# Kernel tuning notes

Measured on AMD Instinct MI355X. Metric: run time of the kernel, lower is better.

Reference implementation:

```python
import jax, jax.numpy as jnp
import numpy as np

A = -0.75  # torch bicubic coefficient
K = 5
K2 = K * K
IN_CH = 32 * 2 + 169 + 16 * 2 + 1  # 266
TIMESTEP = 0.5


def _cubic_w(t):
    # t in [0,1); weights for taps at offsets -1,0,1,2 (torch cubic convolution, A=-0.75)
    w1 = ((A + 2.0) * t - (A + 3.0)) * t * t + 1.0
    s = 1.0 - t
    w2 = ((A + 2.0) * s - (A + 3.0)) * s * s + 1.0
    u = t + 1.0
    w0 = ((A * u - 5.0 * A) * u + 8.0 * A) * u - 4.0 * A
    v = 2.0 - t
    w3 = ((A * v - 5.0 * A) * v + 8.0 * A) * v - 4.0 * A
    return (w0, w1, w2, w3)


def _conv3(x, w, b):
    y = jax.lax.conv_general_dilated(x, w, (1, 1), 'SAME',
                                     dimension_numbers=('NCHW', 'OIHW', 'NCHW'))
    return y + b[None, :, None, None]


def _lrelu(x):
    return jnp.where(x >= 0, x, 0.1 * x)


def _kernel_pred(x, w1, b1, w2, b2, w3, b3, ow, ob, ww, wb):
    f = _lrelu(_conv3(x, w1, b1))
    f = _lrelu(_conv3(f, w2, b2))
    f = _lrelu(_conv3(f, w3, b3))
    offsets = _conv3(f, ow, ob)                      # (B, 2*K2, H, W)
    weights = jax.nn.softmax(_conv3(f, ww, wb), axis=1)  # (B, K2, H, W)
    return offsets, weights


def _adacof_sample(image, offsets, weights):
    # bicubic grid_sample(padding_mode='border', align_corners=True) + weighted combine
    b, c, h, w = image.shape
    k2 = weights.shape[1]
    gx = jnp.arange(w, dtype=image.dtype)
    gy = jnp.arange(h, dtype=image.dtype)
    dx = offsets[:, 0::2]                # (b,k2,h,w)
    dy = offsets[:, 1::2]
    # with align_corners=True, normalize->unnormalize is identity
    sx = gx[None, None, None, :] + dx
    sy = gy[None, None, :, None] + dy
    x0 = jnp.floor(sx); tx = sx - x0
    y0 = jnp.floor(sy); ty = sy - y0
    wx = _cubic_w(tx)
    wy = _cubic_w(ty)
    xi = [jnp.clip(x0 + (i - 1.0), 0, w - 1).astype(jnp.int32) for i in range(4)]
    yi = [jnp.clip(y0 + (i - 1.0), 0, h - 1).astype(jnp.int32) for i in range(4)]
    imgf = image.reshape(b, c, h * w)
    gather = jax.vmap(lambda im, idx: im[:, idx])   # (c,hw),(n,)->(c,n)
    acc = jnp.zeros((b, c, k2, h, w), image.dtype)
    for i in range(4):
        for j in range(4):
            idx = (yi[i] * w + xi[j]).reshape(b, -1)
            g = gather(imgf, idx).reshape(b, c, k2, h, w)
            acc = acc + g * (wy[i] * wx[j])[:, None]
    return jnp.einsum('bckhw,bkhw->bchw', acc, weights)


def setup_inputs() -> dict:
    key = jax.random.key(0)
    ks = iter(jax.random.split(key, 64))
    d = {}
    d['frame1'] = jax.random.normal(next(ks), (2, 3, 256, 256), jnp.float32)
    d['frame2'] = jax.random.normal(next(ks), (2, 3, 256, 256), jnp.float32)
    d['feat1'] = jax.random.normal(next(ks), (2, 32, 256, 256), jnp.float32)
    d['feat2'] = jax.random.normal(next(ks), (2, 32, 256, 256), jnp.float32)
    d['corr'] = jax.random.normal(next(ks), (2, 169, 256, 256), jnp.float32)

    def conv_w(o, i):
        return jax.random.normal(next(ks), (o, i, 3, 3), jnp.float32) * 0.05

    # full-res encoder
    d['fr_w1'] = conv_w(16, 3); d['fr_b1'] = jnp.zeros((16,), jnp.float32)
    d['fr_w2'] = conv_w(16, 16); d['fr_b2'] = jnp.zeros((16,), jnp.float32)
    # default grid offsets for offset_head bias (dx,dy interleaved)
    off_bias = []
    for i in range(K):
        for j in range(K):
            off_bias.extend([j - K // 2, i - K // 2])
    off_bias = jnp.asarray(off_bias, jnp.float32)
    for p in ('kp1', 'kp2'):
        d[p + '_w1'] = conv_w(256, IN_CH); d[p + '_b1'] = jnp.zeros((256,), jnp.float32)
        d[p + '_w2'] = conv_w(256, 256); d[p + '_b2'] = jnp.zeros((256,), jnp.float32)
        d[p + '_w3'] = conv_w(128, 256); d[p + '_b3'] = jnp.zeros((128,), jnp.float32)
        d[p + '_ow'] = jax.random.normal(next(ks), (2 * K2, 128, 3, 3), jnp.float32) * 0.01
        d[p + '_ob'] = off_bias
        d[p + '_ww'] = jax.random.normal(next(ks), (K2, 128, 3, 3), jnp.float32) * 0.01
        d[p + '_wb'] = jnp.full((K2,), 1.0 / K2, jnp.float32)
    d['bl_w1'] = conv_w(64, IN_CH); d['bl_b1'] = jnp.zeros((64,), jnp.float32)
    d['bl_w2'] = conv_w(1, 64); d['bl_b2'] = jnp.zeros((1,), jnp.float32)
    return d


def reference(frame1, frame2, feat1, feat2, corr,
              fr_w1, fr_b1, fr_w2, fr_b2,
              kp1_w1, kp1_b1, kp1_w2, kp1_b2, kp1_w3, kp1_b3, kp1_ow, kp1_ob, kp1_ww, kp1_wb,
              kp2_w1, kp2_b1, kp2_w2, kp2_b2, kp2_w3, kp2_b3, kp2_ow, kp2_ob, kp2_ww, kp2_wb,
              bl_w1, bl_b1, bl_w2, bl_b2):
    b, _, h, w = frame1.shape
    fr1 = _lrelu(_conv3(_lrelu(_conv3(frame1, fr_w1, fr_b1)), fr_w2, fr_b2))
    fr2 = _lrelu(_conv3(_lrelu(_conv3(frame2, fr_w1, fr_b1)), fr_w2, fr_b2))
    t_map = jnp.full((b, 1, h, w), TIMESTEP, frame1.dtype)
    combined = jnp.concatenate([feat1, feat2, corr, fr1, fr2, t_map], axis=1)
    offsets1, weights1 = _kernel_pred(combined, kp1_w1, kp1_b1, kp1_w2, kp1_b2,
                                      kp1_w3, kp1_b3, kp1_ow, kp1_ob, kp1_ww, kp1_wb)
    offsets2, weights2 = _kernel_pred(combined, kp2_w1, kp2_b1, kp2_w2, kp2_b2,
                                      kp2_w3, kp2_b3, kp2_ow, kp2_ob, kp2_ww, kp2_wb)
    sample1 = _adacof_sample(frame1, offsets1, weights1)
    sample2 = _adacof_sample(frame2, offsets2, weights2)
    blend = jax.nn.sigmoid(_conv3(_lrelu(_conv3(combined, bl_w1, bl_b1)), bl_w2, bl_b2))
    output = blend * sample1 + (1.0 - blend) * sample2
    return (output, blend, offsets1, offsets2, weights1, weights2)
```

## Files before the change

kernel.cpp:

```cpp
#include <hip/hip_runtime.h>
#include <cstdint>
#include <cstddef>

#define H 256
#define W 256
#define HW (H*W)
#define BATCH 2
#define CIN_TILE 4

typedef __bf16 bf16x8 __attribute__((ext_vector_type(8)));
typedef float f32x4 __attribute__((ext_vector_type(4)));
typedef __attribute__((address_space(1))) uint32_t gu32_t;
typedef __attribute__((address_space(3))) uint32_t lu32_t;

__device__ __forceinline__ void async16(const void* g, void* l) {
  __builtin_amdgcn_global_load_lds((const gu32_t*)g, (lu32_t*)l, 16, 0, 0);
}

__device__ __forceinline__ ushort f2bf(float f) {
  uint u = __float_as_uint(f);
  return (ushort)((u + 0x7FFFu + ((u >> 16) & 1u)) >> 16);
}
__device__ __forceinline__ float lrelu_f(float v) { return v >= 0.f ? v : 0.1f * v; }

#define SWN (2304 * 8)
#define SBN (4 * 640 * 8)
#define DYN_LDS_BYTES (2 * (SWN + SBN) * 2)

template<int EPI>
__global__ __launch_bounds__(512) void convmm_k(
    const ushort* __restrict__ act, const ushort* __restrict__ wgt,
    const float* __restrict__ bias, ushort* __restrict__ dstb,
    float* __restrict__ dsto, float* __restrict__ dstw,
    const ushort* __restrict__ zpage, int Cin, int CoutS,
    int astride, int wstride, int bstride, int dstride)
{
  extern __shared__ __align__(16) ushort s_dyn[];

  const int z = blockIdx.z;
  act += (size_t)z * astride;
  wgt += (size_t)z * wstride;
  bias += (size_t)z * bstride;
  if constexpr (EPI == 0) dstb += (size_t)z * dstride;
  else { dsto += (size_t)z * (BATCH * 50 * HW); dstw += (size_t)z * (BATCH * 25 * HW); }

  const int tid = threadIdx.x;
  const int sp = blockIdx.x;
  const int bx = (sp & 7) * 32, by = (sp >> 3) * 16;
  const int co0 = blockIdx.y * 64;
  const int wv = tid >> 6, lane = tid & 63;
  const int c = lane & 15, kq = lane >> 4;
  const int oy = wv * 2;

  int wsrc[5];
#pragma unroll
  for (int it = 0; it < 5; ++it) {
    int i = tid + it * 512;
    if (i < 2304) {
      int co = i & 63, tk = i >> 6, tap = tk >> 2, kg = tk & 3;
      wsrc[it] = ((co0 + co) * 9 + tap) * Cin + kg * 8;
    } else wsrc[it] = 0;
  }
  int bsrc[5];
#pragma unroll
  for (int it = 0; it < 5; ++it) {
    int i = tid + it * 512;
    int kg = i / 640, px = i - kg * 640;
    int row = px / 34, xx = px - row * 34;
    int gy = by + row - 1, gx = bx + xx - 1;
    bool ok = (px < 612) && ((unsigned)gy < (unsigned)H) && ((unsigned)gx < (unsigned)W);
    bsrc[it] = ok ? ((gy * W + gx) * Cin + kg * 8) : -1;
  }

  auto stage = [&](int buf, int c0) {
    ushort* swc = s_dyn + (buf ? (SWN + SBN) : 0);
    ushort* sbc = swc + SWN;
#pragma unroll
    for (int it = 0; it < 5; ++it)
      if (it < 4 || tid < 2304 - 4 * 512)
        async16(wgt + wsrc[it] + c0, &swc[(size_t)(tid + it * 512) * 8]);
#pragma unroll
    for (int it = 0; it < 5; ++it) {
      const ushort* g = (bsrc[it] < 0) ? zpage : (act + bsrc[it] + c0);
      async16(g, &sbc[(size_t)(tid + it * 512) * 8]);
    }
  };

  f32x4 acc[4][4];
#pragma unroll
  for (int a = 0; a < 4; ++a)
#pragma unroll
    for (int b2 = 0; b2 < 4; ++b2) acc[a][b2] = (f32x4){0.f, 0.f, 0.f, 0.f};

  stage(0, 0);
  __syncthreads();

  const int nch = Cin >> 5;
  int cur = 0;
  for (int ch = 0; ch < nch; ++ch) {
    if (ch + 1 < nch) stage(cur ^ 1, (ch + 1) << 5);

    const ushort* swc = s_dyn + (cur ? (SWN + SBN) : 0);
    const ushort* sbc = swc + SWN;

#pragma unroll
    for (int t = 0; t < 9; ++t) {
      const int dy = t / 3 - 1, dx = t % 3 - 1;
      bf16x8 B[4];
#pragma unroll
      for (int pf = 0; pf < 4; ++pf) {
        int p = (oy + (pf >> 1) + dy + 1) * 34 + (pf & 1) * 16 + dx + 1 + c;
        B[pf] = *(const bf16x8*)&sbc[(size_t)(kq * 640 + p) * 8];
      }
#pragma unroll
      for (int cf = 0; cf < 4; ++cf) {
        bf16x8 A = *(const bf16x8*)&swc[(size_t)((t * 4 + kq) * 64 + cf * 16 + c) * 8];
#pragma unroll
        for (int pf = 0; pf < 4; ++pf)
          acc[cf][pf] = __builtin_amdgcn_mfma_f32_16x16x32_bf16(A, B[pf], acc[cf][pf], 0, 0, 0);
      }
    }

    __syncthreads();
    cur ^= 1;
  }

  const int r4 = kq * 4;
#pragma unroll
  for (int cf = 0; cf < 4; ++cf) {
    int cob = co0 + cf * 16 + r4;
#pragma unroll
    for (int pf = 0; pf < 4; ++pf) {
      int gx2 = bx + (pf & 1) * 16 + c;
      int gy2 = by + oy + (pf >> 1);
      int gpix = gy2 * W + gx2;
      f32x4 v = acc[cf][pf];
      const float4 bv = *(const float4*)&bias[cob];
      if constexpr (EPI == 0) {
        ushort4 ov;
        float f0 = lrelu_f(v[0] + bv.x);
        float f1 = lrelu_f(v[1] + bv.y);
        float f2 = lrelu_f(v[2] + bv.z);
        float f3 = lrelu_f(v[3] + bv.w);
        ov.x = f2bf(f0); ov.y = f2bf(f1); ov.z = f2bf(f2); ov.w = f2bf(f3);
        *(ushort4*)&dstb[(size_t)gpix * CoutS + cob] = ov;
      } else {
        const float* bvp = &bv.x;
#pragma unroll
        for (int r = 0; r < 4; ++r) {
          int coa = cob + r;
          if (coa < 75) {
            float f = v[r] + bvp[r];
            if (coa < 50) dsto[(size_t)coa * HW + gpix] = f;
            else          dstw[(size_t)(coa - 50) * HW + gpix] = f;
          }
        }
      }
    }
  }
}

template<int CIN>
__global__ __launch_bounds__(256) void conv_fr_k(
    const float* __restrict__ sA, const float* __restrict__ sB, int mode,
    const float* __restrict__ wgt, const float* __restrict__ bias,
    float* __restrict__ dst)
{
  const int z = blockIdx.y;
  const float* src = (mode == 0)
      ? (((z >> 1) ? sB : sA) + (size_t)(z & 1) * 3 * HW)
      : (sA + (size_t)z * 16 * HW);
  float* out = dst + (size_t)z * 16 * HW;

  const int sp = blockIdx.x;
  const int bx = (sp & 7) * 32, by = (sp >> 3) * 32;
  const int tid = threadIdx.x;
  const int tx = tid & 15, ty = tid >> 4;

  __shared__ float s_in[CIN_TILE][34][36];
  float acc[16][2][2];
#pragma unroll
  for (int co = 0; co < 16; ++co) {
    acc[co][0][0] = 0.f; acc[co][0][1] = 0.f;
    acc[co][1][0] = 0.f; acc[co][1][1] = 0.f;
  }

  for (int c0 = 0; c0 < CIN; c0 += CIN_TILE) {
    __syncthreads();
    const int nst = CIN_TILE * 34 * 34;
    for (int i = tid; i < nst; i += 256) {
      int ci = i / (34 * 34);
      int r = i - ci * (34 * 34);
      int yy = r / 34;
      int xx = r - yy * 34;
      int gy = by + yy - 1, gx = bx + xx - 1;
      int cc = c0 + ci;
      float v = 0.f;
      if (cc < CIN && (unsigned)gy < (unsigned)H && (unsigned)gx < (unsigned)W)
        v = src[(size_t)cc * HW + gy * W + gx];
      s_in[ci][yy][xx] = v;
    }
    __syncthreads();

    const int cmax = (CIN - c0 < CIN_TILE) ? (CIN - c0) : CIN_TILE;
    for (int ci = 0; ci < cmax; ++ci) {
      float win[4][4];
#pragma unroll
      for (int iy = 0; iy < 4; ++iy)
#pragma unroll
        for (int ix = 0; ix < 4; ++ix)
          win[iy][ix] = s_in[ci][2 * ty + iy][2 * tx + ix];
#pragma unroll
      for (int co = 0; co < 16; ++co) {
        const float* wp = wgt + ((size_t)co * CIN + (c0 + ci)) * 9;
        float w0 = wp[0], w1 = wp[1], w2 = wp[2];
        float w3 = wp[3], w4 = wp[4], w5 = wp[5];
        float w6 = wp[6], w7 = wp[7], w8 = wp[8];
#pragma unroll
        for (int py = 0; py < 2; ++py)
#pragma unroll
          for (int px = 0; px < 2; ++px) {
            float s = acc[co][py][px];
            s += w0 * win[py + 0][px + 0];
            s += w1 * win[py + 0][px + 1];
            s += w2 * win[py + 0][px + 2];
            s += w3 * win[py + 1][px + 0];
            s += w4 * win[py + 1][px + 1];
            s += w5 * win[py + 1][px + 2];
            s += w6 * win[py + 2][px + 0];
            s += w7 * win[py + 2][px + 1];
            s += w8 * win[py + 2][px + 2];
            acc[co][py][px] = s;
          }
      }
    }
  }
#pragma unroll
  for (int co = 0; co < 16; ++co) {
    float bv = bias[co];
#pragma unroll
    for (int py = 0; py < 2; ++py)
#pragma unroll
      for (int px = 0; px < 2; ++px)
        out[(size_t)co * HW + (size_t)(by + 2 * ty + py) * W + (bx + 2 * tx + px)] =
            lrelu_f(acc[co][py][px] + bv);
  }
}

__global__ __launch_bounds__(256) void pack_k(
    const float* __restrict__ feat1, const float* __restrict__ feat2,
    const float* __restrict__ corr, const float* __restrict__ fr,
    ushort* __restrict__ comb, int b)
{
  int gid = blockIdx.x * 256 + threadIdx.x;
  int chunk = gid / HW;
  int p = gid - chunk * HW;
  int c0 = chunk * 32;

  uint u[16];
#pragma unroll
  for (int j = 0; j < 32; j += 2) {
    float f[2];
#pragma unroll
    for (int q = 0; q < 2; ++q) {
      int cc = c0 + j + q;
      float v;
      if (cc < 32)       v = feat1[(size_t)(b * 32 + cc) * HW + p];
      else if (cc < 64)  v = feat2[(size_t)(b * 32 + cc - 32) * HW + p];
      else if (cc < 233) v = corr[(size_t)(b * 169 + cc - 64) * HW + p];
      else if (cc < 249) v = fr[(size_t)(b * 16 + (cc - 233)) * HW + p];
      else if (cc < 265) v = fr[(size_t)((2 + b) * 16 + (cc - 249)) * HW + p];
      else if (cc == 265) v = 0.5f;
      else               v = 0.f;
      f[q] = v;
    }
    u[j >> 1] = (uint)f2bf(f[0]) | ((uint)f2bf(f[1]) << 16);
  }
  uint4* dst = (uint4*)&comb[(size_t)p * 288 + c0];
#pragma unroll
  for (int q = 0; q < 4; ++q) {
    uint4 t;
    t.x = u[q * 4 + 0]; t.y = u[q * 4 + 1]; t.z = u[q * 4 + 2]; t.w = u[q * 4 + 3];
    dst[q] = t;
  }
}

struct PrepSeg { const float* src; ushort* dst; int O, I, Ipad; };
struct PrepArgs { PrepSeg s[13]; int pre[14]; };

__global__ __launch_bounds__(256) void prep_all_k(PrepArgs a)
{
  int gid = blockIdx.x * 256 + threadIdx.x;
  if (gid >= a.pre[13]) return;
  int si = 0;
  while (gid >= a.pre[si + 1]) ++si;
  int idx = gid - a.pre[si];
  const PrepSeg sg = a.s[si];
  int i = idx % sg.Ipad;
  int r = idx / sg.Ipad;
  int tap = r % 9;
  int o = r / 9;
  float v = (i < sg.I) ? sg.src[((size_t)o * sg.I + i) * 9 + tap] : 0.f;
  sg.dst[idx] = f2bf(v);
}

__global__ __launch_bounds__(256) void bias_all_k(
    const float* kb1_0, const float* kb1_1, const float* kb2_0, const float* kb2_1,
    const float* kb3_0, const float* kb3_1,
    const float* ob0, const float* wb0, const float* ob1, const float* wb1,
    float* bb1, float* bb2, float* bb3, float* bbh)
{
  int yq = blockIdx.y;
  int i = threadIdx.x;
  switch (yq) {
    case 0: bb1[i] = kb1_0[i]; break;
    case 1: bb1[256 + i] = kb1_1[i]; break;
    case 2: bb2[i] = kb2_0[i]; break;
    case 3: bb2[256 + i] = kb2_1[i]; break;
    case 4: if (i < 128) bb3[i] = kb3_0[i]; break;
    case 5: if (i < 128) bb3[128 + i] = kb3_1[i]; break;
    case 6: if (i < 128) bbh[i]       = (i < 50) ? ob0[i] : ((i < 75) ? wb0[i - 50] : 0.f); break;
    case 7: if (i < 128) bbh[128 + i] = (i < 50) ? ob1[i] : ((i < 75) ? wb1[i - 50] : 0.f); break;
  }
}

__global__ __launch_bounds__(256) void blend2_k(
    const ushort* __restrict__ actD, const float* __restrict__ wgt,
    const float* __restrict__ b2, float* __restrict__ outp)
{
  int p = blockIdx.x * 256 + threadIdx.x;
  int y = p >> 8, x = p & 255;
  float acc = b2[0];
  for (int dy = -1; dy <= 1; ++dy) {
    int gy = y + dy;
    if ((unsigned)gy >= (unsigned)H) continue;
    for (int dx = -1; dx <= 1; ++dx) {
      int gx = x + dx;
      if ((unsigned)gx >= (unsigned)W) continue;
      int tap = (dy + 1) * 3 + (dx + 1);
      const ushort* rowp = actD + (size_t)(gy * W + gx) * 64;
#pragma unroll
      for (int c8 = 0; c8 < 8; ++c8) {
        uint4 v = *(const uint4*)&rowp[c8 * 8];
        const uint* vv = &v.x;
#pragma unroll
        for (int q = 0; q < 4; ++q) {
          float f0 = __uint_as_float(vv[q] << 16);
          float f1 = __uint_as_float(vv[q] & 0xFFFF0000u);
          int ci = c8 * 8 + q * 2;
          acc += f0 * wgt[ci * 9 + tap];
          acc += f1 * wgt[(ci + 1) * 9 + tap];
        }
      }
    }
  }
  outp[p] = 1.f / (1.f + expf(-acc));
}

__global__ __launch_bounds__(256) void softmax25_k(float* __restrict__ w1,
                                                   float* __restrict__ w2)
{
  float* wr = blockIdx.y ? w2 : w1;
  int p = blockIdx.x * 256 + threadIdx.x;
  if (p >= HW) return;
  float v[25];
  float m = -1e30f;
#pragma unroll
  for (int k = 0; k < 25; ++k) {
    v[k] = wr[(size_t)k * HW + p];
    m = fmaxf(m, v[k]);
  }
  float s = 0.f;
#pragma unroll
  for (int k = 0; k < 25; ++k) {
    v[k] = expf(v[k] - m);
    s += v[k];
  }
  float inv = 1.f / s;
#pragma unroll
  for (int k = 0; k < 25; ++k)
    wr[(size_t)k * HW + p] = v[k] * inv;
}

__device__ __forceinline__ void cubic4(float t, float* cw)
{
  const float A_ = -0.75f;
  float t2 = t * t;
  cw[1] = ((A_ + 2.f) * t - (A_ + 3.f)) * t2 + 1.f;
  float s = 1.f - t;
  cw[2] = ((A_ + 2.f) * s - (A_ + 3.f)) * (s * s) + 1.f;
  float u = t + 1.f;
  cw[0] = ((A_ * u - 5.f * A_) * u + 8.f * A_) * u - 4.f * A_;
  float v = 2.f - t;
  cw[3] = ((A_ * v - 5.f * A_) * v + 8.f * A_) * v - 4.f * A_;
}

#define ATW 64
#define ATH 4
#define AHL 8
#define AROWS (ATH + 2*AHL)
#define ACOLS (ATW + 2*AHL)

__global__ __launch_bounds__(256) void adacof_final_k(
    const float* __restrict__ frame1, const float* __restrict__ frame2,
    const float* __restrict__ off1, const float* __restrict__ off2,
    const float* __restrict__ wt1, const float* __restrict__ wt2,
    const float* __restrict__ blend, float* __restrict__ outp)
{
  __shared__ __align__(16) float4 s_img[2 * AROWS * ACOLS];

  const int tid = threadIdx.x;
  int t = blockIdx.x;
  const int tilesPerImg = (H / ATH) * (W / ATW);
  const int b = t / tilesPerImg; t -= b * tilesPerImg;
  const int by = (t >> 2) * ATH, bx = (t & 3) * ATW;
  const int ty = tid >> 6, txx = tid & 63;
  const int y = by + ty, x = bx + txx;
  const int p = y * W + x;
  const int tx0 = bx - AHL, ty0 = by - AHL;

  const float* f1 = frame1 + (size_t)b * 3 * HW;
  const float* f2 = frame2 + (size_t)b * 3 * HW;

  for (int i = tid; i < AROWS * ACOLS; i += 256) {
    int r = i / ACOLS, cc = i - r * ACOLS;
    int gy = min(max(ty0 + r, 0), H - 1);
    int gx = min(max(tx0 + cc, 0), W - 1);
    int q = gy * W + gx;
    float4 v1, v2;
    v1.x = f1[q]; v1.y = f1[HW + q]; v1.z = f1[2 * HW + q]; v1.w = 0.f;
    v2.x = f2[q]; v2.y = f2[HW + q]; v2.z = f2[2 * HW + q]; v2.w = 0.f;
    s_img[i] = v1;
    s_img[AROWS * ACOLS + i] = v2;
  }
  __syncthreads();

  float a1[3] = {0.f, 0.f, 0.f};
  float a2[3] = {0.f, 0.f, 0.f};

  const size_t ob1 = (size_t)b * 50 * HW, wb1 = (size_t)b * 25 * HW;

#pragma unroll 2
  for (int k = 0; k < 25; ++k) {
#pragma unroll
    for (int fr = 0; fr < 2; ++fr) {
      const float* off = fr ? off2 : off1;
      const float* wts = fr ? wt2 : wt1;
      const float* img = fr ? f2 : f1;
      float* acc = fr ? a2 : a1;

      float dx = off[ob1 + (size_t)(2 * k) * HW + p];
      float dy = off[ob1 + (size_t)(2 * k + 1) * HW + p];
      float wk = wts[wb1 + (size_t)k * HW + p];
      float sx = (float)x + dx, sy = (float)y + dy;
      float x0f = floorf(sx), y0f = floorf(sy);
      float tx = sx - x0f, tyf = sy - y0f;
      float wx[4], wy[4];
      cubic4(tx, wx);
      cubic4(tyf, wy);
      int ix0 = (int)x0f, iy0 = (int)y0f;

      bool inT = (ix0 - 1 >= tx0) && (ix0 + 2 <= tx0 + ACOLS - 1) &&
                 (iy0 - 1 >= ty0) && (iy0 + 2 <= ty0 + AROWS - 1);
      if (__builtin_expect(inT, 1)) {
        const float4* base = &s_img[(size_t)fr * AROWS * ACOLS +
                                    (iy0 - 1 - ty0) * ACOLS + (ix0 - 1 - tx0)];
#pragma unroll
        for (int i = 0; i < 4; ++i) {
#pragma unroll
          for (int j = 0; j < 4; ++j) {
            float wf = wy[i] * wx[j] * wk;
            float4 v = base[i * ACOLS + j];
            acc[0] += v.x * wf;
            acc[1] += v.y * wf;
            acc[2] += v.z * wf;
          }
        }
      } else {
        int xi[4], yi[4];
#pragma unroll
        for (int i = 0; i < 4; ++i) {
          xi[i] = min(max(ix0 + i - 1, 0), W - 1);
          yi[i] = min(max(iy0 + i - 1, 0), H - 1);
        }
#pragma unroll
        for (int i = 0; i < 4; ++i) {
#pragma unroll
          for (int j = 0; j < 4; ++j) {
            float wf = wy[i] * wx[j] * wk;
            int q = yi[i] * W + xi[j];
            acc[0] += img[q] * wf;
            acc[1] += img[HW + q] * wf;
            acc[2] += img[2 * HW + q] * wf;
          }
        }
      }
    }
  }

  float bl = blend[(size_t)b * HW + p];
#pragma unroll
  for (int c3 = 0; c3 < 3; ++c3)
    outp[((size_t)b * 3 + c3) * HW + p] = bl * a1[c3] + (1.f - bl) * a2[c3];
}

extern "C" void kernel_launch(void* const* d_in, const int* in_sizes, int n_in,
                              void* d_out, int out_size, void* d_ws, size_t ws_size,
                              hipStream_t stream)
{
  const float* frame1 = (const float*)d_in[0];
  const float* frame2 = (const float*)d_in[1];
  const float* feat1  = (const float*)d_in[2];
  const float* feat2  = (const float*)d_in[3];
  const float* corr   = (const float*)d_in[4];
  const float* fr_w1  = (const float*)d_in[5];
  const float* fr_b1  = (const float*)d_in[6];
  const float* fr_w2  = (const float*)d_in[7];
  const float* fr_b2  = (const float*)d_in[8];

  const float* kw1[2] = {(const float*)d_in[9],  (const float*)d_in[19]};
  const float* kb1[2] = {(const float*)d_in[10], (const float*)d_in[20]};
  const float* kw2[2] = {(const float*)d_in[11], (const float*)d_in[21]};
  const float* kb2[2] = {(const float*)d_in[12], (const float*)d_in[22]};
  const float* kw3[2] = {(const float*)d_in[13], (const float*)d_in[23]};
  const float* kb3[2] = {(const float*)d_in[14], (const float*)d_in[24]};
  const float* kow[2] = {(const float*)d_in[15], (const float*)d_in[25]};
  const float* kob[2] = {(const float*)d_in[16], (const float*)d_in[26]};
  const float* kww[2] = {(const float*)d_in[17], (const float*)d_in[27]};
  const float* kwb[2] = {(const float*)d_in[18], (const float*)d_in[28]};

  const float* bl_w1 = (const float*)d_in[29];
  const float* bl_b1 = (const float*)d_in[30];
  const float* bl_w2 = (const float*)d_in[31];
  const float* bl_b2 = (const float*)d_in[32];

  float* out = (float*)d_out;
  float* o_out   = out;
  float* o_blend = o_out   + (size_t)BATCH * 3 * HW;
  float* o_off1  = o_blend + (size_t)BATCH * 1 * HW;
  float* o_off2  = o_off1  + (size_t)BATCH * 50 * HW;
  float* o_w1    = o_off2  + (size_t)BATCH * 50 * HW;
  float* o_w2    = o_w1    + (size_t)BATCH * 25 * HW;

  hipFuncSetAttribute((const void*)convmm_k<0>,
                      hipFuncAttributeMaxDynamicSharedMemorySize, DYN_LDS_BYTES);
  hipFuncSetAttribute((const void*)convmm_k<1>,
                      hipFuncAttributeMaxDynamicSharedMemorySize, DYN_LDS_BYTES);

  size_t off = 0;
  char* wsb = (char*)d_ws;
  auto alloc = [&](size_t bytes) -> void* {
    void* pp = wsb + off;
    off += (bytes + 255) & ~(size_t)255;
    return pp;
  };
  const size_t NEED_MERGED = 212700000;
  const bool merged = ws_size >= NEED_MERGED;
  const int NZ = merged ? 2 : 1;

  ushort* zpage = (ushort*)alloc(512);
  ushort* wp1   = (ushort*)alloc((size_t)2 * 256 * 9 * 288 * 2);
  ushort* wp2   = (ushort*)alloc((size_t)2 * 256 * 9 * 256 * 2);
  ushort* wp3   = (ushort*)alloc((size_t)2 * 128 * 9 * 256 * 2);
  ushort* wph   = (ushort*)alloc((size_t)2 * 128 * 9 * 128 * 2);
  ushort* wpb   = (ushort*)alloc((size_t)64 * 9 * 288 * 2);
  float*  bb1   = (float*)alloc(2 * 256 * 4);
  float*  bb2   = (float*)alloc(2 * 256 * 4);
  float*  bb3   = (float*)alloc(2 * 128 * 4);
  float*  bbh   = (float*)alloc(2 * 128 * 4);
  float*  tmp4  = (float*)alloc((size_t)4 * 16 * HW * 4);
  float*  frbuf = (float*)alloc((size_t)4 * 16 * HW * 4);
  ushort* comb  = (ushort*)alloc((size_t)HW * 288 * 2);
  ushort* actA  = (ushort*)alloc((size_t)NZ * HW * 256 * 2);
  ushort* actB  = (ushort*)alloc((size_t)NZ * HW * 256 * 2);

  dim3 blk(256);
  dim3 cblk(512);

  hipMemsetAsync(zpage, 0, 512, stream);
  {
    PrepArgs pa;
    const int W1 = 256 * 9 * 288, W2 = 256 * 9 * 256, W3 = 128 * 9 * 256;
    const int OW = 50 * 9 * 128, WW = 25 * 9 * 128, ZW = 53 * 9 * 128;
    const int WB = 64 * 9 * 288;
    const int HP = 128 * 9 * 128;
    PrepSeg segs[13] = {
      {kw1[0], wp1,                    256, 266, 288},
      {kw1[1], wp1 + W1,               256, 266, 288},
      {kw2[0], wp2,                    256, 256, 256},
      {kw2[1], wp2 + W2,               256, 256, 256},
      {kw3[0], wp3,                    128, 256, 256},
      {kw3[1], wp3 + W3,               128, 256, 256},
      {kow[0], wph,                     50, 128, 128},
      {kww[0], wph + OW,                25, 128, 128},
      {nullptr, wph + OW + WW,          53,   0, 128},
      {kow[1], wph + HP,                50, 128, 128},
      {kww[1], wph + HP + OW,           25, 128, 128},
      {nullptr, wph + HP + OW + WW,     53,   0, 128},
      {bl_w1,  wpb,                     64, 266, 288},
    };
    int tots[13] = {W1, W1, W2, W2, W3, W3, OW, WW, ZW, OW, WW, ZW, WB};
    pa.pre[0] = 0;
    for (int s = 0; s < 13; ++s) { pa.s[s] = segs[s]; pa.pre[s + 1] = pa.pre[s] + tots[s]; }
    int nblk = (pa.pre[13] + 255) / 256;
    prep_all_k<<<dim3(nblk), blk, 0, stream>>>(pa);
  }
  bias_all_k<<<dim3(1, 8), blk, 0, stream>>>(kb1[0], kb1[1], kb2[0], kb2[1],
                                             kb3[0], kb3[1], kob[0], kwb[0],
                                             kob[1], kwb[1], bb1, bb2, bb3, bbh);

  conv_fr_k<3><<<dim3(64, 4), blk, 0, stream>>>(frame1, frame2, 0, fr_w1, fr_b1, tmp4);
  conv_fr_k<16><<<dim3(64, 4), blk, 0, stream>>>(tmp4, nullptr, 1, fr_w2, fr_b2, frbuf);

  const int W1 = 256 * 9 * 288, W2 = 256 * 9 * 256, W3 = 128 * 9 * 256;
  const int HP = 128 * 9 * 128;

  for (int b = 0; b < BATCH; ++b) {
    pack_k<<<dim3(9 * HW / 256), blk, 0, stream>>>(feat1, feat2, corr, frbuf, comb, b);

    for (int pp = 0; pp < 2 / NZ; ++pp) {
      const size_t po = pp;
      convmm_k<0><<<dim3(128, 4, NZ), cblk, DYN_LDS_BYTES, stream>>>(
          comb, wp1 + po * W1, bb1 + po * 256, actA + po * (size_t)HW * 256,
          nullptr, nullptr, zpage, 288, 256, 0, W1, 256, HW * 256);
      convmm_k<0><<<dim3(128, 4, NZ), cblk, DYN_LDS_BYTES, stream>>>(
          actA + po * (size_t)HW * 256, wp2 + po * W2, bb2 + po * 256,
          actB + po * (size_t)HW * 256,
          nullptr, nullptr, zpage, 256, 256, HW * 256, W2, 256, HW * 256);
      convmm_k<0><<<dim3(128, 2, NZ), cblk, DYN_LDS_BYTES, stream>>>(
          actB + po * (size_t)HW * 256, wp3 + po * W3, bb3 + po * 128,
          actA + po * (size_t)HW * 128,
          nullptr, nullptr, zpage, 256, 128, HW * 256, W3, 128, HW * 128);
      convmm_k<1><<<dim3(128, 2, NZ), cblk, DYN_LDS_BYTES, stream>>>(
          actA + po * (size_t)HW * 128, wph + po * HP, bbh + po * 128, nullptr,
          o_off1 + (size_t)b * 50 * HW + po * (size_t)BATCH * 50 * HW,
          o_w1 + (size_t)b * 25 * HW + po * (size_t)BATCH * 25 * HW,
          zpage, 128, 0, HW * 128, HP, 128, 0);
    }
    softmax25_k<<<dim3(HW / 256, 2), blk, 0, stream>>>(
        o_w1 + (size_t)b * 25 * HW, o_w2 + (size_t)b * 25 * HW);

    convmm_k<0><<<dim3(128, 1, 1), cblk, DYN_LDS_BYTES, stream>>>(
        comb, wpb, bl_b1, actB, nullptr, nullptr, zpage, 288, 64, 0, 0, 0, 0);
    blend2_k<<<dim3(HW / 256), blk, 0, stream>>>(actB, bl_w2, bl_b2,
                                                 o_blend + (size_t)b * HW);
  }

  adacof_final_k<<<dim3(BATCH * (H / ATH) * (W / ATW)), blk, 0, stream>>>(
      frame1, frame2, o_off1, o_off2, o_w1, o_w2, o_blend, o_out);
}
```

Before: 1.331 ms.

## Software-pipeline LDS fragment reads across taps with inline asm and setprio

Replaces the compiler-scheduled LDS loads in the conv implicit-GEMM inner loop with hand-issued ds_read_b128 instructions. They use precomputed base addresses and immediate tap offsets, and the A/B fragments are double-buffered in registers so the reads for tap t+1 are in flight while the MFMAs for tap t run. Manual lgkmcnt waits and sched_barriers enforce the ordering, and s_setprio raises wave priority around the MFMA burst. The aim is to hide LDS latency and cut address arithmetic. The cost is higher register pressure and fragile manual synchronization that the compiler can no longer reorder.

```diff
diff --git a/kernel.cpp b/kernel.cpp
--- a/kernel.cpp
+++ b/kernel.cpp
@@ -26,6 +26,30 @@
 #define SWN (2304 * 8)
 #define SBN (4 * 640 * 8)
 #define DYN_LDS_BYTES (2 * (SWN + SBN) * 2)
+
+#define ISSUE_TAP(tt, bb)                                                     \
+  do {                                                                        \
+    asm volatile("ds_read_b128 %0, %1 offset:%c2"                             \
+                 : "=v"(Afr[bb][0]) : "v"(aA0), "i"((tt) * 4096));            \
+    asm volatile("ds_read_b128 %0, %1 offset:%c2"                             \
+                 : "=v"(Afr[bb][1]) : "v"(aA1), "i"((tt) * 4096));            \
+    asm volatile("ds_read_b128 %0, %1 offset:%c2"                             \
+                 : "=v"(Afr[bb][2]) : "v"(aA2), "i"((tt) * 4096));            \
+    asm volatile("ds_read_b128 %0, %1 offset:%c2"                             \
+                 : "=v"(Afr[bb][3]) : "v"(aA3), "i"((tt) * 4096));            \
+    asm volatile("ds_read_b128 %0, %1 offset:%c2"                             \
+                 : "=v"(Bfr[bb][0]) : "v"(aB0),                               \
+                   "i"(((((tt) / 3) * 34) + ((tt) % 3)) * 16));               \
+    asm volatile("ds_read_b128 %0, %1 offset:%c2"                             \
+                 : "=v"(Bfr[bb][1]) : "v"(aB1),                               \
+                   "i"(((((tt) / 3) * 34) + ((tt) % 3)) * 16));               \
+    asm volatile("ds_read_b128 %0, %1 offset:%c2"                             \
+                 : "=v"(Bfr[bb][2]) : "v"(aB2),                               \
+                   "i"(((((tt) / 3) * 34) + ((tt) % 3)) * 16));               \
+    asm volatile("ds_read_b128 %0, %1 offset:%c2"                             \
+                 : "=v"(Bfr[bb][3]) : "v"(aB3),                               \
+                   "i"(((((tt) / 3) * 34) + ((tt) % 3)) * 16));               \
+  } while (0)
 
 template<int EPI>
 __global__ __launch_bounds__(512) void convmm_k(
@@ -95,30 +119,56 @@
   stage(0, 0);
   __syncthreads();
 
+  const uint sdyn_base = (uint)(uintptr_t)(lu32_t*)s_dyn;
+
   const int nch = Cin >> 5;
   int cur = 0;
   for (int ch = 0; ch < nch; ++ch) {
     if (ch + 1 < nch) stage(cur ^ 1, (ch + 1) << 5);
-
-    const ushort* swc = s_dyn + (cur ? (SWN + SBN) : 0);
-    const ushort* sbc = swc + SWN;
+    __builtin_amdgcn_sched_barrier(0);
+
+    const uint swoff = sdyn_base + (cur ? (uint)((SWN + SBN) * 2) : 0u);
+    const uint sboff = swoff + (uint)(SWN * 2);
+    const uint aA0 = swoff + (uint)((kq * 64 + 0 * 16 + c) * 16);
+    const uint aA1 = swoff + (uint)((kq * 64 + 1 * 16 + c) * 16);
+    const uint aA2 = swoff + (uint)((kq * 64 + 2 * 16 + c) * 16);
+    const uint aA3 = swoff + (uint)((kq * 64 + 3 * 16 + c) * 16);
+    const uint aB0 = sboff + (uint)((kq * 640 + (oy + 0) * 34 + 0 * 16 + c) * 16);
+    const uint aB1 = sboff + (uint)((kq * 640 + (oy + 0) * 34 + 1 * 16 + c) * 16);
+    const uint aB2 = sboff + (uint)((kq * 640 + (oy + 1) * 34 + 0 * 16 + c) * 16);
+    const uint aB3 = sboff + (uint)((kq * 640 + (oy + 1) * 34 + 1 * 16 + c) * 16);
+
+    bf16x8 Afr[2][4], Bfr[2][4];
+    ISSUE_TAP(0, 0);
 
 #pragma unroll
     for (int t = 0; t < 9; ++t) {
-      const int dy = t / 3 - 1, dx = t % 3 - 1;
-      bf16x8 B[4];
-#pragma unroll
-      for (int pf = 0; pf < 4; ++pf) {
-        int p = (oy + (pf >> 1) + dy + 1) * 34 + (pf & 1) * 16 + dx + 1 + c;
-        B[pf] = *(const bf16x8*)&sbc[(size_t)(kq * 640 + p) * 8];
+      if (t < 8) {
+        switch (t + 1) {
+          case 1: ISSUE_TAP(1, 1); break;
+          case 2: ISSUE_TAP(2, 0); break;
+          case 3: ISSUE_TAP(3, 1); break;
+          case 4: ISSUE_TAP(4, 0); break;
+          case 5: ISSUE_TAP(5, 1); break;
+          case 6: ISSUE_TAP(6, 0); break;
+          case 7: ISSUE_TAP(7, 1); break;
+          case 8: ISSUE_TAP(8, 0); break;
+        }
+        asm volatile("s_waitcnt lgkmcnt(8)" ::: "memory");
+      } else {
+        asm volatile("s_waitcnt lgkmcnt(0)" ::: "memory");
       }
+      __builtin_amdgcn_sched_barrier(0);
+      __builtin_amdgcn_s_setprio(1);
 #pragma unroll
       for (int cf = 0; cf < 4; ++cf) {
-        bf16x8 A = *(const bf16x8*)&swc[(size_t)((t * 4 + kq) * 64 + cf * 16 + c) * 8];
 #pragma unroll
         for (int pf = 0; pf < 4; ++pf)
-          acc[cf][pf] = __builtin_amdgcn_mfma_f32_16x16x32_bf16(A, B[pf], acc[cf][pf], 0, 0, 0);
+          acc[cf][pf] = __builtin_amdgcn_mfma_f32_16x16x32_bf16(
+              Afr[t & 1][cf], Bfr[t & 1][pf], acc[cf][pf], 0, 0, 0);
       }
+      __builtin_amdgcn_s_setprio(0);
+      __builtin_amdgcn_sched_barrier(0);
     }
 
     __syncthreads();
```

Result: faster. 1.302 ms (median of 2 runs) (-2.2%).

## Widen conv implicit-GEMM tile to 128 output channels with single-buffered weights

Applied to the files above, without the earlier changes.

The conv GEMM kernel now computes 128 output channels per block instead of 64. The eight waves are split into four row groups and two channel groups, each holding an 8-pixel-fragment accumulator. The aim is to raise arithmetic intensity and reuse of the activation tile in LDS, and to halve the grid in the channel dimension. Weights are now single-buffered and loaded after the compute sync, which adds a second barrier per chunk and exposes weight load latency. Accumulator register pressure doubles, and the blend conv weights are zero-padded to 128 channels, spending MFMA work on unused channels.

```diff
diff --git a/kernel.cpp b/kernel.cpp
--- a/kernel.cpp
+++ b/kernel.cpp
@@ -23,12 +23,12 @@
 }
 __device__ __forceinline__ float lrelu_f(float v) { return v >= 0.f ? v : 0.1f * v; }
 
-#define SWN (2304 * 8)
-#define SBN (4 * 640 * 8)
-#define DYN_LDS_BYTES (2 * (SWN + SBN) * 2)
+#define WGTU (4608 * 8)
+#define SBU  (2560 * 8)
+#define DYN_LDS_BYTES ((WGTU + 2 * SBU) * 2)
 
 template<int EPI>
-__global__ __launch_bounds__(512) void convmm_k(
+__global__ __launch_bounds__(512, 2) void convmm_k(
     const ushort* __restrict__ act, const ushort* __restrict__ wgt,
     const float* __restrict__ bias, ushort* __restrict__ dstb,
     float* __restrict__ dsto, float* __restrict__ dstw,
@@ -36,6 +36,7 @@
     int astride, int wstride, int bstride, int dstride)
 {
   extern __shared__ __align__(16) ushort s_dyn[];
+  ushort* const swc = s_dyn;
 
   const int z = blockIdx.z;
   act += (size_t)z * astride;
@@ -47,19 +48,18 @@
   const int tid = threadIdx.x;
   const int sp = blockIdx.x;
   const int bx = (sp & 7) * 32, by = (sp >> 3) * 16;
-  const int co0 = blockIdx.y * 64;
+  const int co0 = blockIdx.y * 128;
   const int wv = tid >> 6, lane = tid & 63;
   const int c = lane & 15, kq = lane >> 4;
-  const int oy = wv * 2;
-
-  int wsrc[5];
-#pragma unroll
-  for (int it = 0; it < 5; ++it) {
+  const int wr = wv & 3, cg = wv >> 2;
+
+  int wsrc[9];
+#pragma unroll
+  for (int it = 0; it < 9; ++it) {
     int i = tid + it * 512;
-    if (i < 2304) {
-      int co = i & 63, tk = i >> 6, tap = tk >> 2, kg = tk & 3;
-      wsrc[it] = ((co0 + co) * 9 + tap) * Cin + kg * 8;
-    } else wsrc[it] = 0;
+    int co = i & 127, tk = i >> 7;
+    int tap = tk >> 2, kg = tk & 3;
+    wsrc[it] = ((co0 + co) * 9 + tap) * Cin + kg * 8;
   }
   int bsrc[5];
 #pragma unroll
@@ -72,13 +72,13 @@
     bsrc[it] = ok ? ((gy * W + gx) * Cin + kg * 8) : -1;
   }
 
-  auto stage = [&](int buf, int c0) {
-    ushort* swc = s_dyn + (buf ? (SWN + SBN) : 0);
-    ushort* sbc = swc + SWN;
-#pragma unroll
-    for (int it = 0; it < 5; ++it)
-      if (it < 4 || tid < 2304 - 4 * 512)
-        async16(wgt + wsrc[it] + c0, &swc[(size_t)(tid + it * 512) * 8]);
+  auto stage_wgt = [&](int c0) {
+#pragma unroll
+    for (int it = 0; it < 9; ++it)
+      async16(wgt + wsrc[it] + c0, &swc[(size_t)(tid + it * 512) * 8]);
+  };
+  auto stage_act = [&](int buf, int c0) {
+    ushort* sbc = s_dyn + WGTU + buf * SBU;
 #pragma unroll
     for (int it = 0; it < 5; ++it) {
       const ushort* g = (bsrc[it] < 0) ? zpage : (act + bsrc[it] + c0);
@@ -86,73 +86,87 @@
     }
   };
 
-  f32x4 acc[4][4];
+  f32x4 acc[4][8];
 #pragma unroll
   for (int a = 0; a < 4; ++a)
 #pragma unroll
-    for (int b2 = 0; b2 < 4; ++b2) acc[a][b2] = (f32x4){0.f, 0.f, 0.f, 0.f};
-
-  stage(0, 0);
+    for (int b2 = 0; b2 < 8; ++b2) acc[a][b2] = (f32x4){0.f, 0.f, 0.f, 0.f};
+
+  stage_wgt(0);
+  stage_act(0, 0);
   __syncthreads();
 
   const int nch = Cin >> 5;
   int cur = 0;
   for (int ch = 0; ch < nch; ++ch) {
-    if (ch + 1 < nch) stage(cur ^ 1, (ch + 1) << 5);
-
-    const ushort* swc = s_dyn + (cur ? (SWN + SBN) : 0);
-    const ushort* sbc = swc + SWN;
+    if (ch + 1 < nch) stage_act(cur ^ 1, (ch + 1) << 5);
+    __builtin_amdgcn_sched_barrier(0);
+
+    const ushort* sbc = s_dyn + WGTU + cur * SBU;
 
 #pragma unroll
     for (int t = 0; t < 9; ++t) {
       const int dy = t / 3 - 1, dx = t % 3 - 1;
-      bf16x8 B[4];
-#pragma unroll
-      for (int pf = 0; pf < 4; ++pf) {
-        int p = (oy + (pf >> 1) + dy + 1) * 34 + (pf & 1) * 16 + dx + 1 + c;
-        B[pf] = *(const bf16x8*)&sbc[(size_t)(kq * 640 + p) * 8];
+      bf16x8 Bv[8];
+#pragma unroll
+      for (int pf = 0; pf < 8; ++pf) {
+        int R = wr * 4 + (pf >> 1) + dy + 1;
+        int p = kq * 640 + R * 34 + (pf & 1) * 16 + dx + 1 + c;
+        Bv[pf] = *(const bf16x8*)&sbc[(size_t)p * 8];
       }
 #pragma unroll
       for (int cf = 0; cf < 4; ++cf) {
-        bf16x8 A = *(const bf16x8*)&swc[(size_t)((t * 4 + kq) * 64 + cf * 16 + c) * 8];
-#pragma unroll
-        for (int pf = 0; pf < 4; ++pf)
-          acc[cf][pf] = __builtin_amdgcn_mfma_f32_16x16x32_bf16(A, B[pf], acc[cf][pf], 0, 0, 0);
+        int a = (t * 4 + kq) * 128 + cg * 64 + cf * 16 + c;
+        bf16x8 Av = *(const bf16x8*)&swc[(size_t)a * 8];
+#pragma unroll
+        for (int pf = 0; pf < 8; ++pf)
+          acc[cf][pf] = __builtin_amdgcn_mfma_f32_16x16x32_bf16(
+              Av, Bv[pf], acc[cf][pf], 0, 0, 0);
       }
     }
 
     __syncthreads();
+    if (ch + 1 < nch) {
+      stage_wgt((ch + 1) << 5);
+      __syncthreads();
+    }
     cur ^= 1;
   }
 
   const int r4 = kq * 4;
 #pragma unroll
   for (int cf = 0; cf < 4; ++cf) {
-    int cob = co0 + cf * 16 + r4;
-#pragma unroll
-    for (int pf = 0; pf < 4; ++pf) {
-      int gx2 = bx + (pf & 1) * 16 + c;
-      int gy2 = by + oy + (pf >> 1);
-      int gpix = gy2 * W + gx2;
-      f32x4 v = acc[cf][pf];
-      const float4 bv = *(const float4*)&bias[cob];
-      if constexpr (EPI == 0) {
-        ushort4 ov;
-        float f0 = lrelu_f(v[0] + bv.x);
-        float f1 = lrelu_f(v[1] + bv.y);
-        float f2 = lrelu_f(v[2] + bv.z);
-        float f3 = lrelu_f(v[3] + bv.w);
-        ov.x = f2bf(f0); ov.y = f2bf(f1); ov.z = f2bf(f2); ov.w = f2bf(f3);
-        *(ushort4*)&dstb[(size_t)gpix * CoutS + cob] = ov;
-      } else {
-        const float* bvp = &bv.x;
-#pragma unroll
-        for (int r = 0; r < 4; ++r) {
-          int coa = cob + r;
-          if (coa < 75) {
-            float f = v[r] + bvp[r];
-            if (coa < 50) dsto[(size_t)coa * HW + gpix] = f;
-            else          dstw[(size_t)(coa - 50) * HW + gpix] = f;
+    int cob = co0 + cg * 64 + cf * 16 + r4;
+    if (cob < CoutS || EPI == 1) {
+#pragma unroll
+      for (int pf = 0; pf < 8; ++pf) {
+        int gx2 = bx + (pf & 1) * 16 + c;
+        int gy2 = by + wr * 4 + (pf >> 1);
+        int gpix = gy2 * W + gx2;
+        f32x4 v = acc[cf][pf];
+        if constexpr (EPI == 0) {
+          const float4 bv = *(const float4*)&bias[cob];
+          ushort4 ov;
+          float f0 = lrelu_f(v[0] + bv.x);
+          float f1 = lrelu_f(v[1] + bv.y);
+          float f2 = lrelu_f(v[2] + bv.z);
+          float f3 = lrelu_f(v[3] + bv.w);
+          ov.x = f2bf(f0); ov.y = f2bf(f1); ov.z = f2bf(f2); ov.w = f2bf(f3);
+          *(ushort4*)&dstb[(size_t)gpix * CoutS + cob] = ov;
+        } else {
+          int cb2 = cg * 64 + cf * 16 + r4;
+          if (cb2 < 75) {
+            const float4 bv = *(const float4*)&bias[cb2];
+            const float* bvp = &bv.x;
+#pragma unroll
+            for (int r = 0; r < 4; ++r) {
+              int coa = cb2 + r;
+              if (coa < 75) {
+                float f = v[r] + bvp[r];
+                if (coa < 50) dsto[(size_t)coa * HW + gpix] = f;
+                else          dstw[(size_t)(coa - 50) * HW + gpix] = f;
+              }
+            }
           }
         }
       }
@@ -286,12 +300,12 @@
 }
 
 struct PrepSeg { const float* src; ushort* dst; int O, I, Ipad; };
-struct PrepArgs { PrepSeg s[13]; int pre[14]; };
+struct PrepArgs { PrepSeg s[14]; int pre[15]; };
 
 __global__ __launch_bounds__(256) void prep_all_k(PrepArgs a)
 {
   int gid = blockIdx.x * 256 + threadIdx.x;
-  if (gid >= a.pre[13]) return;
+  if (gid >= a.pre[14]) return;
   int si = 0;
   while (gid >= a.pre[si + 1]) ++si;
   int idx = gid - a.pre[si];
@@ -563,7 +577,7 @@
   ushort* wp2   = (ushort*)alloc((size_t)2 * 256 * 9 * 256 * 2);
   ushort* wp3   = (ushort*)alloc((size_t)2 * 128 * 9 * 256 * 2);
   ushort* wph   = (ushort*)alloc((size_t)2 * 128 * 9 * 128 * 2);
-  ushort* wpb   = (ushort*)alloc((size_t)64 * 9 * 288 * 2);
+  ushort* wpb   = (ushort*)alloc((size_t)128 * 9 * 288 * 2);
   float*  bb1   = (float*)alloc(2 * 256 * 4);
   float*  bb2   = (float*)alloc(2 * 256 * 4);
   float*  bb3   = (float*)alloc(2 * 128 * 4);
@@ -582,9 +596,9 @@
     PrepArgs pa;
     const int W1 = 256 * 9 * 288, W2 = 256 * 9 * 256, W3 = 128 * 9 * 256;
     const int OW = 50 * 9 * 128, WW = 25 * 9 * 128, ZW = 53 * 9 * 128;
-    const int WB = 64 * 9 * 288;
+    const int WB = 64 * 9 * 288, ZB = 64 * 9 * 288;
     const int HP = 128 * 9 * 128;
-    PrepSeg segs[13] = {
+    PrepSeg segs[14] = {
       {kw1[0], wp1,                    256, 266, 288},
       {kw1[1], wp1 + W1,               256, 266, 288},
       {kw2[0], wp2,                    256, 256, 256},
@@ -598,11 +612,12 @@
       {kww[1], wph + HP + OW,           25, 128, 128},
       {nullptr, wph + HP + OW + WW,     53,   0, 128},
       {bl_w1,  wpb,                     64, 266, 288},
+      {nullptr, wpb + WB,               64,   0, 288},
     };
-    int tots[13] = {W1, W1, W2, W2, W3, W3, OW, WW, ZW, OW, WW, ZW, WB};
+    int tots[14] = {W1, W1, W2, W2, W3, W3, OW, WW, ZW, OW, WW, ZW, WB, ZB};
     pa.pre[0] = 0;
-    for (int s = 0; s < 13; ++s) { pa.s[s] = segs[s]; pa.pre[s + 1] = pa.pre[s] + tots[s]; }
-    int nblk = (pa.pre[13] + 255) / 256;
+    for (int s = 0; s < 14; ++s) { pa.s[s] = segs[s]; pa.pre[s + 1] = pa.pre[s] + tots[s]; }
+    int nblk = (pa.pre[14] + 255) / 256;
     prep_all_k<<<dim3(nblk), blk, 0, stream>>>(pa);
   }
   bias_all_k<<<dim3(1, 8), blk, 0, stream>>>(kb1[0], kb1[1], kb2[0], kb2[1],
@@ -620,18 +635,18 @@
 
     for (int pp = 0; pp < 2 / NZ; ++pp) {
       const size_t po = pp;
-      convmm_k<0><<<dim3(128, 4, NZ), cblk, DYN_LDS_BYTES, stream>>>(
+      convmm_k<0><<<dim3(128, 2, NZ), cblk, DYN_LDS_BYTES, stream>>>(
           comb, wp1 + po * W1, bb1 + po * 256, actA + po * (size_t)HW * 256,
           nullptr, nullptr, zpage, 288, 256, 0, W1, 256, HW * 256);
-      convmm_k<0><<<dim3(128, 4, NZ), cblk, DYN_LDS_BYTES, stream>>>(
+      convmm_k<0><<<dim3(128, 2, NZ), cblk, DYN_LDS_BYTES, stream>>>(
           actA + po * (size_t)HW * 256, wp2 + po * W2, bb2 + po * 256,
           actB + po * (size_t)HW * 256,
           nullptr, nullptr, zpage, 256, 256, HW * 256, W2, 256, HW * 256);
-      convmm_k<0><<<dim3(128, 2, NZ), cblk, DYN_LDS_BYTES, stream>>>(
+      convmm_k<0><<<dim3(128, 1, NZ), cblk, DYN_LDS_BYTES, stream>>>(
           actB + po * (size_t)HW * 256, wp3 + po * W3, bb3 + po * 128,
           actA + po * (size_t)HW * 128,
           nullptr, nullptr, zpage, 256, 128, HW * 256, W3, 128, HW * 128);
-      convmm_k<1><<<dim3(128, 2, NZ), cblk, DYN_LDS_BYTES, stream>>>(
+      convmm_k<1><<<dim3(128, 1, NZ), cblk, DYN_LDS_BYTES, stream>>>(
           actA + po * (size_t)HW * 128, wph + po * HP, bbh + po * 128, nullptr,
           o_off1 + (size_t)b * 50 * HW + po * (size_t)BATCH * 50 * HW,
           o_w1 + (size_t)b * 25 * HW + po * (size_t)BATCH * 25 * HW,
```

New measurement: 1.935 ms. 1.45x slower.
